# Kernel optimization log

Measured on AMD Instinct MI355X. Metric: run time of the kernel, lower is better.

The kernel has to match this reference:

```python
import jax, jax.numpy as jnp
import numpy as np

N_AGENTS, T, B, S = 8, 128, 64, 16
D_STATE, E, HH = 128, 64, 128


def _hyper(x, k1, b1, k2, b2):
    return jax.nn.relu(x @ k1 + b1) @ k2 + b2


def _perm_pos(n_agents, tb, s):
    # pos[row, a] = position of agent a in a random grand-coalition permutation
    keys = jax.random.split(jax.random.key(42), tb * s)
    pos = jax.vmap(lambda k: jax.random.permutation(k, n_agents))(keys)
    return pos.reshape(tb, s, n_agents)


def setup_inputs() -> dict:
    key = jax.random.key(0)
    ks = jax.random.split(key, 12)
    def rn(k, shape, scale=0.05):
        return jax.random.normal(k, shape, jnp.float32) * scale
    return {
        "q_vals": rn(ks[0], (N_AGENTS, T, B), 1.0),
        "states": rn(ks[1], (T * B, D_STATE), 1.0),
        "hw1_k1": rn(ks[2], (D_STATE, HH)), "hw1_b1": jnp.zeros((HH,), jnp.float32),
        "hw1_k2": rn(ks[3], (HH, 2 * E)), "hw1_b2": jnp.zeros((2 * E,), jnp.float32),
        "b1_k": rn(ks[4], (D_STATE, E)), "b1_b": jnp.zeros((E,), jnp.float32),
        "hw2_k1": rn(ks[5], (D_STATE, HH)), "hw2_b1": jnp.zeros((HH,), jnp.float32),
        "hw2_k2": rn(ks[6], (HH, E)), "hw2_b2": jnp.zeros((E,), jnp.float32),
        "hb2_k1": rn(ks[7], (D_STATE, E)), "hb2_b1": jnp.zeros((E,), jnp.float32),
        "hb2_k2": rn(ks[8], (E, 1)), "hb2_b2": jnp.zeros((1,), jnp.float32),
    }


def _forward(pos, q_vals, states, hw1_k1, hw1_b1, hw1_k2, hw1_b2, b1_k, b1_b,
             hw2_k1, hw2_b1, hw2_k2, hw2_b2, hb2_k1, hb2_b1, hb2_k2, hb2_b2):
    n, t, b = q_vals.shape
    tb = t * b
    q = jnp.transpose(q_vals, (1, 2, 0)).reshape(tb, n)          # agent_qs, (tb, n)
    qb = jnp.broadcast_to(q[:, None, :], (tb, S, n))
    inv = jnp.argsort(pos, axis=-1)                               # agent at each position
    q_ord = jnp.take_along_axis(qb, inv, axis=-1)                 # q ordered by position
    csum_excl = jnp.cumsum(q_ord, axis=-1) - q_ord                # sum over strictly-earlier positions
    coal_sum = jnp.take_along_axis(csum_excl, pos, axis=-1)       # sum of preceding agents' q
    coal_norm = coal_sum / jnp.maximum(pos, 1).astype(q.dtype)    # mean (0 if no predecessors)
    # Hypernets depend only on states -> compute once per tb row, broadcast over (S, n)
    w1 = jnp.abs(_hyper(states, hw1_k1, hw1_b1, hw1_k2, hw1_b2)).reshape(tb, 1, 1, 2, E)
    b1 = (states @ b1_k + b1_b).reshape(tb, 1, 1, E)
    w2 = jnp.abs(_hyper(states, hw2_k1, hw2_b1, hw2_k2, hw2_b2)).reshape(tb, 1, 1, E)
    b2 = _hyper(states, hb2_k1, hb2_b1, hb2_k2, hb2_b2).reshape(tb, 1, 1)
    hidden = jax.nn.elu(coal_norm[..., None] * w1[..., 0, :]
                        + qb[..., None] * w1[..., 1, :] + b1)     # (tb, S, n, E)
    y = jnp.sum(hidden * w2, axis=-1) + b2                        # (tb, S, n)
    alpha = jnp.abs(y).reshape(t, b, S, n).mean(axis=2)           # mean over samples
    return jnp.transpose(alpha, (2, 0, 1))                        # (n, t, b)


def reference(q_vals, states, hw1_k1, hw1_b1, hw1_k2, hw1_b2, b1_k, b1_b,
              hw2_k1, hw2_b1, hw2_k2, hw2_b2, hb2_k1, hb2_b1, hb2_k2, hb2_b2):
    n, t, b = q_vals.shape
    pos = _perm_pos(n, t * b, S)
    return _forward(pos, q_vals, states, hw1_k1, hw1_b1, hw1_k2, hw1_b2, b1_k, b1_b,
                    hw2_k1, hw2_b1, hw2_k2, hw2_b2, hb2_k1, hb2_b1, hb2_k2, hb2_b2)
```

## Files before the change

### kernel.cpp

```cpp
#include <hip/hip_runtime.h>
#include <stdint.h>

#define N_AG   8
#define S_SAMP 16
#define TB     8192
#define DST    128
#define E_DIM  64

#define RPB    8
#define CN_STR 9

#define WT1K1  0
#define WT2K1  16384
#define WT1K2  32768
#define WTM3   49152
#define WT2K2  65536
#define WT_ELEMS 73728

typedef __attribute__((ext_vector_type(8))) short  short8v;
typedef __attribute__((ext_vector_type(4))) float  float4v;

__device__ __forceinline__ float4 ld4(const float* p) { return *(const float4*)p; }

__device__ __forceinline__ unsigned short f2bf(float f) {
  uint32_t x = __float_as_uint(f);
  return (unsigned short)((x + 0x7FFFu + ((x >> 16) & 1u)) >> 16);
}
__device__ __forceinline__ uint32_t pk2(float lo, float hi) {
  return (uint32_t)f2bf(lo) | ((uint32_t)f2bf(hi) << 16);
}

__device__ __forceinline__ uint2 tf2x32(uint32_t k0, uint32_t k1,
                                        uint32_t c0, uint32_t c1) {
  uint32_t ks2 = k0 ^ k1 ^ 0x1BD11BDAu;
  uint32_t x0 = c0 + k0, x1 = c1 + k1;
#define TFR(r) { x0 += x1; x1 = (x1 << (r)) | (x1 >> (32 - (r))); x1 ^= x0; }
  TFR(13) TFR(15) TFR(26) TFR(6)
  x0 += k1;  x1 += ks2 + 1u;
  TFR(17) TFR(29) TFR(16) TFR(24)
  x0 += ks2; x1 += k0 + 2u;
  TFR(13) TFR(15) TFR(26) TFR(6)
  x0 += k0;  x1 += k1 + 3u;
  TFR(17) TFR(29) TFR(16) TFR(24)
  x0 += k1;  x1 += ks2 + 4u;
  TFR(13) TFR(15) TFR(26) TFR(6)
  x0 += ks2; x1 += k0 + 5u;
#undef TFR
  return make_uint2(x0, x1);
}

__device__ __forceinline__ short8v rdfrag(const unsigned short* base, int row, int ks, int lhi) {
  const int b = (row * 256 + ks * 64 + lhi * 16) ^ ((row & 7) << 4);
  return *(const short8v*)((const char*)base + b);
}
__device__ __forceinline__ void wrbf(unsigned short* pan, int r, int c, float v) {
  const int b = (r * 256 + c * 2) ^ ((r & 7) << 4);
  *(unsigned short*)((char*)pan + b) = f2bf(v);
}
__device__ __forceinline__ short8v gfrag(const unsigned short* wt, int n, int ks, int lhi) {
  return *(const short8v*)(wt + (n << 7) + ks * 32 + lhi * 8);
}

__global__ __launch_bounds__(256)
void wt_transpose(const float* __restrict__ hw1_k1, const float* __restrict__ hw2_k1,
                  const float* __restrict__ hw1_k2, const float* __restrict__ b1_k,
                  const float* __restrict__ hb2_k1, const float* __restrict__ hw2_k2,
                  unsigned short* __restrict__ wt)
{
  __shared__ float t[32][33];
  const int b = blockIdx.x;
  const float* src; int ldn, t0, dstbase;
  if (b < 16)      { src = hw1_k1; ldn = 128; t0 = b;      dstbase = WT1K1; }
  else if (b < 32) { src = hw2_k1; ldn = 128; t0 = b - 16; dstbase = WT2K1; }
  else if (b < 48) { src = hw1_k2; ldn = 128; t0 = b - 32; dstbase = WT1K2; }
  else if (b < 56) { src = b1_k;   ldn = 64;  t0 = b - 48; dstbase = WTM3; }
  else if (b < 64) { src = hb2_k1; ldn = 64;  t0 = b - 56; dstbase = WTM3 + 64 * 128; }
  else             { src = hw2_k2; ldn = 64;  t0 = b - 64; dstbase = WT2K2; }
  const int kt = t0 & 3, nt = t0 >> 2;
  const int tid = threadIdx.x;
  {
    const int c = tid & 31;
    for (int r = tid >> 5; r < 32; r += 8)
      t[r][c] = src[(size_t)(kt * 32 + r) * ldn + nt * 32 + c];
  }
  __syncthreads();
  {
    const int c2 = tid & 15;
    for (int n = tid >> 4; n < 32; n += 16) {
      const uint32_t v = pk2(t[2 * c2][n], t[2 * c2 + 1][n]);
      *(uint32_t*)&wt[dstbase + (nt * 32 + n) * 128 + kt * 32 + 2 * c2] = v;
    }
  }
}

__global__ __launch_bounds__(256)
void alpha_mfma2(const float* __restrict__ q_vals,
                 const float* __restrict__ states,
                 const float* __restrict__ hw1_b1, const float* __restrict__ hw1_b2,
                 const float* __restrict__ b1_b,   const float* __restrict__ hw2_b1,
                 const float* __restrict__ hw2_b2, const float* __restrict__ hb2_b1,
                 const float* __restrict__ hb2_k2, const float* __restrict__ hb2_b2,
                 const unsigned short* __restrict__ wt,
                 float* __restrict__ out)
{
  __shared__ unsigned short xbf[RPB * 128];
  __shared__ unsigned short h1bf[RPB * 128];
  __shared__ unsigned short h2bf[RPB * 128];
  __shared__ float w1l[RPB][132];
  __shared__ float b1l[RPB][68];
  __shared__ float w2l[RPB][68];
  __shared__ float hbl[RPB][68];
  __shared__ float b2l[RPB];
  __shared__ float ql[RPB][N_AG];
  __shared__ float cn_l[RPB][S_SAMP][CN_STR];

  const int tid  = threadIdx.x;
  const int row0 = blockIdx.x * RPB;
  const int lane = tid & 63;
  const int wv   = tid >> 6;
  const int lrow = lane & 15;
  const int lhi  = lane >> 4;

  {
    const int r = tid >> 5, k0 = (tid & 31) * 4;
    const float4 v = ld4(&states[(size_t)(row0 + r) * DST + k0]);
    const int b = (r * 256 + k0 * 2) ^ ((r & 7) << 4);
    *(uint32_t*)((char*)xbf + b)     = pk2(v.x, v.y);
    *(uint32_t*)((char*)xbf + b + 4) = pk2(v.z, v.w);
  }
  if (tid < RPB * N_AG) {
    const int rr = tid >> 3, a = tid & 7;
    ql[rr][a] = q_vals[a * TB + row0 + rr];
  }
  __syncthreads();

  if (tid < RPB * S_SAMP) {
    const int r  = tid >> 4;
    const int sl = tid & 15;
    const uint32_t j = (uint32_t)(row0 + r) * (uint32_t)S_SAMP + (uint32_t)sl;
    uint2 kj  = tf2x32(0u, 42u, 0u, j);
    uint2 sub = tf2x32(kj.x, kj.y, 0u, 1u);
    uint32_t K[N_AG];
#pragma unroll
    for (int i = 0; i < N_AG; ++i) {
      uint2 b = tf2x32(sub.x, sub.y, 0u, (uint32_t)i);
      K[i] = b.x ^ b.y;
    }
    int posa[N_AG];
#pragma unroll
    for (int i = 0; i < N_AG; ++i) {
      int rank = 0;
#pragma unroll
      for (int m = 0; m < N_AG; ++m)
        rank += (K[m] < K[i]) || (K[m] == K[i] && m < i);
      posa[rank] = i;
    }
#pragma unroll
    for (int a = 0; a < N_AG; ++a) {
      const int pa = posa[a];
      float cs = 0.f;
#pragma unroll
      for (int a2 = 0; a2 < N_AG; ++a2)
        cs += (posa[a2] < pa) ? ql[r][a2] : 0.f;
      cn_l[r][sl][a] = cs / (float)max(pa, 1);
    }
  }

  {
    float4v a0 = {0.f,0.f,0.f,0.f}, a1 = {0.f,0.f,0.f,0.f};
    const int c0 = wv * 32 + lrow, c1 = c0 + 16;
#pragma unroll
    for (int ks = 0; ks < 4; ++ks) {
      const short8v af  = rdfrag(xbf, lrow & 7, ks, lhi);
      const short8v b0  = gfrag(wt + WT1K1, c0, ks, lhi);
      const short8v b1f = gfrag(wt + WT1K1, c1, ks, lhi);
      a0 = __builtin_amdgcn_mfma_f32_16x16x32_bf16(af, b0,  a0, 0, 0, 0);
      a1 = __builtin_amdgcn_mfma_f32_16x16x32_bf16(af, b1f, a1, 0, 0, 0);
    }
    if (lhi < 2) {
      const float bv0 = hw1_b1[c0], bv1 = hw1_b1[c1];
#pragma unroll
      for (int j = 0; j < 4; ++j) {
        const int r = lhi * 4 + j;
        wrbf(h1bf, r, c0, fmaxf(a0[j] + bv0, 0.f));
        wrbf(h1bf, r, c1, fmaxf(a1[j] + bv1, 0.f));
      }
    }
  }

  {
    float4v a0 = {0.f,0.f,0.f,0.f}, a1 = {0.f,0.f,0.f,0.f};
    const int c0 = wv * 32 + lrow, c1 = c0 + 16;
#pragma unroll
    for (int ks = 0; ks < 4; ++ks) {
      const short8v af  = rdfrag(xbf, lrow & 7, ks, lhi);
      const short8v b0  = gfrag(wt + WT2K1, c0, ks, lhi);
      const short8v b1f = gfrag(wt + WT2K1, c1, ks, lhi);
      a0 = __builtin_amdgcn_mfma_f32_16x16x32_bf16(af, b0,  a0, 0, 0, 0);
      a1 = __builtin_amdgcn_mfma_f32_16x16x32_bf16(af, b1f, a1, 0, 0, 0);
    }
    if (lhi < 2) {
      const float bv0 = hw2_b1[c0], bv1 = hw2_b1[c1];
#pragma unroll
      for (int j = 0; j < 4; ++j) {
        const int r = lhi * 4 + j;
        wrbf(h2bf, r, c0, fmaxf(a0[j] + bv0, 0.f));
        wrbf(h2bf, r, c1, fmaxf(a1[j] + bv1, 0.f));
      }
    }
  }

  {
    float4v a0 = {0.f,0.f,0.f,0.f}, a1 = {0.f,0.f,0.f,0.f};
    const int c0 = wv * 32 + lrow, c1 = c0 + 16;
#pragma unroll
    for (int ks = 0; ks < 4; ++ks) {
      const short8v af  = rdfrag(xbf, lrow & 7, ks, lhi);
      const short8v b0  = gfrag(wt + WTM3, c0, ks, lhi);
      const short8v b1f = gfrag(wt + WTM3, c1, ks, lhi);
      a0 = __builtin_amdgcn_mfma_f32_16x16x32_bf16(af, b0,  a0, 0, 0, 0);
      a1 = __builtin_amdgcn_mfma_f32_16x16x32_bf16(af, b1f, a1, 0, 0, 0);
    }
    if (lhi < 2) {
#pragma unroll
      for (int j = 0; j < 4; ++j) {
        const int r = lhi * 4 + j;
        if (c0 < 64) b1l[r][c0] = a0[j] + b1_b[c0];
        else         hbl[r][c0 - 64] = fmaxf(a0[j] + hb2_b1[c0 - 64], 0.f);
        if (c1 < 64) b1l[r][c1] = a1[j] + b1_b[c1];
        else         hbl[r][c1 - 64] = fmaxf(a1[j] + hb2_b1[c1 - 64], 0.f);
      }
    }
  }
  __syncthreads();

  if (tid < RPB * S_SAMP) {
    const int r = tid >> 4, sl = tid & 15;
    float v = hbl[r][sl]      * hb2_k2[sl]
            + hbl[r][sl + 16] * hb2_k2[sl + 16]
            + hbl[r][sl + 32] * hb2_k2[sl + 32]
            + hbl[r][sl + 48] * hb2_k2[sl + 48];
    v += __shfl_down(v, 8, 16); v += __shfl_down(v, 4, 16);
    v += __shfl_down(v, 2, 16); v += __shfl_down(v, 1, 16);
    if (sl == 0) b2l[r] = v + hb2_b2[0];
  }

  {
    float4v a0 = {0.f,0.f,0.f,0.f}, a1 = {0.f,0.f,0.f,0.f};
    const int c0 = wv * 32 + lrow, c1 = c0 + 16;
#pragma unroll
    for (int ks = 0; ks < 4; ++ks) {
      const short8v af  = rdfrag(h1bf, lrow & 7, ks, lhi);
      const short8v b0  = gfrag(wt + WT1K2, c0, ks, lhi);
      const short8v b1f = gfrag(wt + WT1K2, c1, ks, lhi);
      a0 = __builtin_amdgcn_mfma_f32_16x16x32_bf16(af, b0,  a0, 0, 0, 0);
      a1 = __builtin_amdgcn_mfma_f32_16x16x32_bf16(af, b1f, a1, 0, 0, 0);
    }
    if (lhi < 2) {
      const float bv0 = hw1_b2[c0], bv1 = hw1_b2[c1];
#pragma unroll
      for (int j = 0; j < 4; ++j) {
        const int r = lhi * 4 + j;
        w1l[r][c0] = fabsf(a0[j] + bv0);
        w1l[r][c1] = fabsf(a1[j] + bv1);
      }
    }
  }

  {
    float4v a0 = {0.f,0.f,0.f,0.f};
    const int c = wv * 16 + lrow;
#pragma unroll
    for (int ks = 0; ks < 4; ++ks) {
      const short8v af = rdfrag(h2bf, lrow & 7, ks, lhi);
      const short8v b0 = gfrag(wt + WT2K2, c, ks, lhi);
      a0 = __builtin_amdgcn_mfma_f32_16x16x32_bf16(af, b0, a0, 0, 0, 0);
    }
    if (lhi < 2) {
      const float bv = hw2_b2[c];
#pragma unroll
      for (int j = 0; j < 4; ++j)
        w2l[lhi * 4 + j][c] = fabsf(a0[j] + bv);
    }
  }
  __syncthreads();

  {
    const int sl = tid & 15;
    const int r  = (tid >> 4) & 7;
    const int a0i = (tid >> 7) * 4;
    float cn[4], qv[4], y[4];
#pragma unroll
    for (int jj = 0; jj < 4; ++jj) {
      cn[jj] = cn_l[r][sl][a0i + jj];
      qv[jj] = ql[r][a0i + jj];
      y[jj]  = 0.f;
    }
#pragma unroll 4
    for (int e = 0; e < E_DIM; e += 4) {
      const float4 wa  = ld4(&w1l[r][e]);
      const float4 wb  = ld4(&w1l[r][64 + e]);
      const float4 bb  = ld4(&b1l[r][e]);
      const float4 w2v = ld4(&w2l[r][e]);
#pragma unroll
      for (int jj = 0; jj < 4; ++jj) {
        float h;
        h = fmaf(cn[jj], wa.x, fmaf(qv[jj], wb.x, bb.x));
        y[jj] = fmaf((h > 0.f) ? h : (__expf(h) - 1.f), w2v.x, y[jj]);
        h = fmaf(cn[jj], wa.y, fmaf(qv[jj], wb.y, bb.y));
        y[jj] = fmaf((h > 0.f) ? h : (__expf(h) - 1.f), w2v.y, y[jj]);
        h = fmaf(cn[jj], wa.z, fmaf(qv[jj], wb.z, bb.z));
        y[jj] = fmaf((h > 0.f) ? h : (__expf(h) - 1.f), w2v.z, y[jj]);
        h = fmaf(cn[jj], wa.w, fmaf(qv[jj], wb.w, bb.w));
        y[jj] = fmaf((h > 0.f) ? h : (__expf(h) - 1.f), w2v.w, y[jj]);
      }
    }
    const float b2v = b2l[r];
#pragma unroll
    for (int jj = 0; jj < 4; ++jj)
      cn_l[r][sl][a0i + jj] = fabsf(y[jj] + b2v);
  }
  __syncthreads();

  if (tid < RPB * N_AG) {
    const int rr = tid & 7, a = tid >> 3;
    float acc = 0.f;
#pragma unroll
    for (int ss = 0; ss < S_SAMP; ++ss) acc += cn_l[rr][ss][a];
    out[a * TB + row0 + rr] = acc * (1.0f / (float)S_SAMP);
  }
}

#define FB_RPB 16
#define FB_H_PAD 132
#define FB_E_PAD 68
__global__ __launch_bounds__(256)
void alpha_fused2(const float* __restrict__ q_vals, const float* __restrict__ states,
                  const float* __restrict__ hw1_k1, const float* __restrict__ hw1_b1,
                  const float* __restrict__ hw1_k2, const float* __restrict__ hw1_b2,
                  const float* __restrict__ b1_k,   const float* __restrict__ b1_b,
                  const float* __restrict__ hw2_k1, const float* __restrict__ hw2_b1,
                  const float* __restrict__ hw2_k2, const float* __restrict__ hw2_b2,
                  const float* __restrict__ hb2_k1, const float* __restrict__ hb2_b1,
                  const float* __restrict__ hb2_k2, const float* __restrict__ hb2_b2,
                  float* __restrict__ out)
{
  __shared__ float s_lds[FB_RPB][DST];
  __shared__ float scratch[FB_RPB][FB_H_PAD];
  __shared__ float scratch2[FB_RPB][FB_E_PAD];
  __shared__ float w1l[FB_RPB][FB_H_PAD];
  __shared__ float b1l[FB_RPB][FB_E_PAD];
  __shared__ float w2l[FB_RPB][FB_E_PAD];
  __shared__ float b2l[FB_RPB];
  __shared__ float qlf[FB_RPB][N_AG];
  __shared__ float cnred[FB_RPB][S_SAMP][N_AG];
  const int tid = threadIdx.x;
  const int row0 = blockIdx.x * FB_RPB;
  const int r = tid >> 4, sl = tid & 15;
  {
    const float4* src = reinterpret_cast<const float4*>(states + (size_t)row0 * DST);
    reinterpret_cast<float4*>(&s_lds[0][0])[tid]       = src[tid];
    reinterpret_cast<float4*>(&s_lds[0][0])[tid + 256] = src[tid + 256];
  }
  if (tid < FB_RPB * N_AG) {
    const int rr = tid >> 3, a = tid & 7;
    qlf[rr][a] = q_vals[a * TB + row0 + rr];
  }
  __syncthreads();
  {
    const uint32_t j = (uint32_t)(row0 + r) * (uint32_t)S_SAMP + (uint32_t)sl;
    uint2 kj = tf2x32(0u, 42u, 0u, j);
    uint2 sub = tf2x32(kj.x, kj.y, 0u, 1u);
    uint32_t K[N_AG];
#pragma unroll
    for (int i = 0; i < N_AG; ++i) { uint2 b = tf2x32(sub.x, sub.y, 0u, (uint32_t)i); K[i] = b.x ^ b.y; }
    int posa[N_AG];
#pragma unroll
    for (int i = 0; i < N_AG; ++i) {
      int rank = 0;
#pragma unroll
      for (int m = 0; m < N_AG; ++m) rank += (K[m] < K[i]) || (K[m] == K[i] && m < i);
      posa[rank] = i;
    }
#pragma unroll
    for (int a = 0; a < N_AG; ++a) {
      const int pa = posa[a];
      float cs = 0.f;
#pragma unroll
      for (int a2 = 0; a2 < N_AG; ++a2) cs += (posa[a2] < pa) ? qlf[r][a2] : 0.f;
      cnred[r][sl][a] = cs / (float)max(pa, 1);
    }
  }
#define FB128(SRC, W, BIAS, DSTA, ACT)                                          \
  {                                                                             \
    const int c = tid & 127, gg = tid >> 7;                                     \
    float a0 = 0.f, a1 = 0.f, a2 = 0.f, a3 = 0.f;                               \
    _Pragma("unroll 2") for (int k = 0; k < DST; k += 4) {                      \
      const float w0 = W[(k + 0) * 128 + c];                                    \
      const float w1 = W[(k + 1) * 128 + c];                                    \
      const float w2 = W[(k + 2) * 128 + c];                                    \
      const float w3 = W[(k + 3) * 128 + c];                                    \
      float4 v;                                                                 \
      v = ld4(&SRC[gg * 8 + 0][0] + k);                                         \
      a0 = fmaf(v.x, w0, a0); a0 = fmaf(v.y, w1, a0);                           \
      a0 = fmaf(v.z, w2, a0); a0 = fmaf(v.w, w3, a0);                           \
      v = ld4(&SRC[gg * 8 + 1][0] + k);                                         \
      a1 = fmaf(v.x, w0, a1); a1 = fmaf(v.y, w1, a1);                           \
      a1 = fmaf(v.z, w2, a1); a1 = fmaf(v.w, w3, a1);                           \
      v = ld4(&SRC[gg * 8 + 2][0] + k);                                         \
      a2 = fmaf(v.x, w0, a2); a2 = fmaf(v.y, w1, a2);                           \
      a2 = fmaf(v.z, w2, a2); a2 = fmaf(v.w, w3, a2);                           \
      v = ld4(&SRC[gg * 8 + 3][0] + k);                                         \
      a3 = fmaf(v.x, w0, a3); a3 = fmaf(v.y, w1, a3);                           \
      a3 = fmaf(v.z, w2, a3); a3 = fmaf(v.w, w3, a3);                           \
      v = ld4(&SRC[gg * 8 + 4][0] + k);                                         \
      DSTA[gg * 8 + 4][c] = 0.f;             \
      (void)v;                                                                  \
    }                                                                           \
    (void)a0; (void)a1; (void)a2; (void)a3; (void)BIAS; (void)ACT;              \
  }
#undef FB128
  {
    int c = tid & 127, rg = tid >> 7;
    float a0=0.f,a1=0.f,a2=0.f,a3=0.f,a4=0.f,a5=0.f,a6=0.f,a7=0.f;
#pragma unroll 2
    for (int k = 0; k < DST; ++k) {
      float wv = hw1_k1[k * 128 + c];
      a0 += s_lds[rg*8+0][k]*wv; a1 += s_lds[rg*8+1][k]*wv;
      a2 += s_lds[rg*8+2][k]*wv; a3 += s_lds[rg*8+3][k]*wv;
      a4 += s_lds[rg*8+4][k]*wv; a5 += s_lds[rg*8+5][k]*wv;
      a6 += s_lds[rg*8+6][k]*wv; a7 += s_lds[rg*8+7][k]*wv;
    }
    float b = hw1_b1[c];
    scratch[rg*8+0][c]=fmaxf(a0+b,0.f); scratch[rg*8+1][c]=fmaxf(a1+b,0.f);
    scratch[rg*8+2][c]=fmaxf(a2+b,0.f); scratch[rg*8+3][c]=fmaxf(a3+b,0.f);
    scratch[rg*8+4][c]=fmaxf(a4+b,0.f); scratch[rg*8+5][c]=fmaxf(a5+b,0.f);
    scratch[rg*8+6][c]=fmaxf(a6+b,0.f); scratch[rg*8+7][c]=fmaxf(a7+b,0.f);
  }
  {
    int c = tid & 63, rg = tid >> 6;
    float a0=0.f,a1=0.f,a2=0.f,a3=0.f;
#pragma unroll 2
    for (int k = 0; k < DST; ++k) {
      float wv = b1_k[k * 64 + c];
      a0 += s_lds[rg*4+0][k]*wv; a1 += s_lds[rg*4+1][k]*wv;
      a2 += s_lds[rg*4+2][k]*wv; a3 += s_lds[rg*4+3][k]*wv;
    }
    float b = b1_b[c];
    b1l[rg*4+0][c]=a0+b; b1l[rg*4+1][c]=a1+b; b1l[rg*4+2][c]=a2+b; b1l[rg*4+3][c]=a3+b;
  }
  __syncthreads();
  {
    int c = tid & 127, rg = tid >> 7;
    float a0=0.f,a1=0.f,a2=0.f,a3=0.f,a4=0.f,a5=0.f,a6=0.f,a7=0.f;
#pragma unroll 2
    for (int k = 0; k < DST; ++k) {
      float wv = hw1_k2[k * 128 + c];
      a0 += scratch[rg*8+0][k]*wv; a1 += scratch[rg*8+1][k]*wv;
      a2 += scratch[rg*8+2][k]*wv; a3 += scratch[rg*8+3][k]*wv;
      a4 += scratch[rg*8+4][k]*wv; a5 += scratch[rg*8+5][k]*wv;
      a6 += scratch[rg*8+6][k]*wv; a7 += scratch[rg*8+7][k]*wv;
    }
    float b = hw1_b2[c];
    w1l[rg*8+0][c]=fabsf(a0+b); w1l[rg*8+1][c]=fabsf(a1+b);
    w1l[rg*8+2][c]=fabsf(a2+b); w1l[rg*8+3][c]=fabsf(a3+b);
    w1l[rg*8+4][c]=fabsf(a4+b); w1l[rg*8+5][c]=fabsf(a5+b);
    w1l[rg*8+6][c]=fabsf(a6+b); w1l[rg*8+7][c]=fabsf(a7+b);
  }
  {
    int c = tid & 63, rg = tid >> 6;
    float a0=0.f,a1=0.f,a2=0.f,a3=0.f;
#pragma unroll 2
    for (int k = 0; k < DST; ++k) {
      float wv = hb2_k1[k * 64 + c];
      a0 += s_lds[rg*4+0][k]*wv; a1 += s_lds[rg*4+1][k]*wv;
      a2 += s_lds[rg*4+2][k]*wv; a3 += s_lds[rg*4+3][k]*wv;
    }
    float b = hb2_b1[c];
    scratch2[rg*4+0][c]=fmaxf(a0+b,0.f); scratch2[rg*4+1][c]=fmaxf(a1+b,0.f);
    scratch2[rg*4+2][c]=fmaxf(a2+b,0.f); scratch2[rg*4+3][c]=fmaxf(a3+b,0.f);
  }
  __syncthreads();
  {
    int c = tid & 127, rg = tid >> 7;
    float a0=0.f,a1=0.f,a2=0.f,a3=0.f,a4=0.f,a5=0.f,a6=0.f,a7=0.f;
#pragma unroll 2
    for (int k = 0; k < DST; ++k) {
      float wv = hw2_k1[k * 128 + c];
      a0 += s_lds[rg*8+0][k]*wv; a1 += s_lds[rg*8+1][k]*wv;
      a2 += s_lds[rg*8+2][k]*wv; a3 += s_lds[rg*8+3][k]*wv;
      a4 += s_lds[rg*8+4][k]*wv; a5 += s_lds[rg*8+5][k]*wv;
      a6 += s_lds[rg*8+6][k]*wv; a7 += s_lds[rg*8+7][k]*wv;
    }
    float b = hw2_b1[c];
    scratch[rg*8+0][c]=fmaxf(a0+b,0.f); scratch[rg*8+1][c]=fmaxf(a1+b,0.f);
    scratch[rg*8+2][c]=fmaxf(a2+b,0.f); scratch[rg*8+3][c]=fmaxf(a3+b,0.f);
    scratch[rg*8+4][c]=fmaxf(a4+b,0.f); scratch[rg*8+5][c]=fmaxf(a5+b,0.f);
    scratch[rg*8+6][c]=fmaxf(a6+b,0.f); scratch[rg*8+7][c]=fmaxf(a7+b,0.f);
  }
  if (tid < FB_RPB * S_SAMP) {
    float v = scratch2[r][sl]      * hb2_k2[sl]
            + scratch2[r][sl + 16] * hb2_k2[sl + 16]
            + scratch2[r][sl + 32] * hb2_k2[sl + 32]
            + scratch2[r][sl + 48] * hb2_k2[sl + 48];
    v += __shfl_down(v, 8, 16); v += __shfl_down(v, 4, 16);
    v += __shfl_down(v, 2, 16); v += __shfl_down(v, 1, 16);
    if (sl == 0) b2l[r] = v + hb2_b2[0];
  }
  __syncthreads();
  {
    int c = tid & 63, rg = tid >> 6;
    float a0=0.f,a1=0.f,a2=0.f,a3=0.f;
#pragma unroll 2
    for (int k = 0; k < DST; ++k) {
      float wv = hw2_k2[k * 64 + c];
      a0 += scratch[rg*4+0][k]*wv; a1 += scratch[rg*4+1][k]*wv;
      a2 += scratch[rg*4+2][k]*wv; a3 += scratch[rg*4+3][k]*wv;
    }
    float b = hw2_b2[c];
    w2l[rg*4+0][c]=fabsf(a0+b); w2l[rg*4+1][c]=fabsf(a1+b);
    w2l[rg*4+2][c]=fabsf(a2+b); w2l[rg*4+3][c]=fabsf(a3+b);
  }
  __syncthreads();
  {
    float cn[N_AG], qv[N_AG], y[N_AG];
#pragma unroll
    for (int a = 0; a < N_AG; ++a) { cn[a]=cnred[r][sl][a]; qv[a]=qlf[r][a]; y[a]=0.f; }
#pragma unroll 4
    for (int e = 0; e < E_DIM; e += 4) {
      const float4 wa  = ld4(&w1l[r][e]);
      const float4 wb  = ld4(&w1l[r][64 + e]);
      const float4 bb  = ld4(&b1l[r][e]);
      const float4 w2v = ld4(&w2l[r][e]);
#pragma unroll
      for (int a = 0; a < N_AG; ++a) {
        float h;
        h = fmaf(cn[a], wa.x, fmaf(qv[a], wb.x, bb.x));
        y[a] = fmaf((h > 0.f) ? h : (__expf(h) - 1.f), w2v.x, y[a]);
        h = fmaf(cn[a], wa.y, fmaf(qv[a], wb.y, bb.y));
        y[a] = fmaf((h > 0.f) ? h : (__expf(h) - 1.f), w2v.y, y[a]);
        h = fmaf(cn[a], wa.z, fmaf(qv[a], wb.z, bb.z));
        y[a] = fmaf((h > 0.f) ? h : (__expf(h) - 1.f), w2v.z, y[a]);
        h = fmaf(cn[a], wa.w, fmaf(qv[a], wb.w, bb.w));
        y[a] = fmaf((h > 0.f) ? h : (__expf(h) - 1.f), w2v.w, y[a]);
      }
    }
    const float b2v = b2l[r];
#pragma unroll
    for (int a = 0; a < N_AG; ++a) cnred[r][sl][a] = fabsf(y[a] + b2v);
  }
  __syncthreads();
  if (tid < FB_RPB * N_AG) {
    const int a = tid >> 4, rr = tid & 15;
    float acc = 0.f;
#pragma unroll
    for (int ss = 0; ss < S_SAMP; ++ss) acc += cnred[rr][ss][a];
    out[a * TB + row0 + rr] = acc * (1.0f / (float)S_SAMP);
  }
}

extern "C" void kernel_launch(void* const* d_in, const int* in_sizes, int n_in,
                              void* d_out, int out_size, void* d_ws, size_t ws_size,
                              hipStream_t stream) {
  const float* q_vals = (const float*)d_in[0];
  const float* states = (const float*)d_in[1];
  const float* hw1_k1 = (const float*)d_in[2];
  const float* hw1_b1 = (const float*)d_in[3];
  const float* hw1_k2 = (const float*)d_in[4];
  const float* hw1_b2 = (const float*)d_in[5];
  const float* b1_k   = (const float*)d_in[6];
  const float* b1_b   = (const float*)d_in[7];
  const float* hw2_k1 = (const float*)d_in[8];
  const float* hw2_b1 = (const float*)d_in[9];
  const float* hw2_k2 = (const float*)d_in[10];
  const float* hw2_b2 = (const float*)d_in[11];
  const float* hb2_k1 = (const float*)d_in[12];
  const float* hb2_b1 = (const float*)d_in[13];
  const float* hb2_k2 = (const float*)d_in[14];
  const float* hb2_b2 = (const float*)d_in[15];
  float* out = (float*)d_out;

  const size_t need = (size_t)WT_ELEMS * sizeof(unsigned short);
  if (ws_size >= need) {
    unsigned short* wt = (unsigned short*)d_ws;
    wt_transpose<<<dim3(72), 256, 0, stream>>>(
        hw1_k1, hw2_k1, hw1_k2, b1_k, hb2_k1, hw2_k2, wt);
    alpha_mfma2<<<dim3(TB / RPB), 256, 0, stream>>>(
        q_vals, states, hw1_b1, hw1_b2, b1_b, hw2_b1, hw2_b2, hb2_b1,
        hb2_k2, hb2_b2, wt, out);
  } else {
    alpha_fused2<<<dim3(TB / FB_RPB), 256, 0, stream>>>(
        q_vals, states, hw1_k1, hw1_b1, hw1_k2, hw1_b2, b1_k, b1_b,
        hw2_k1, hw2_b1, hw2_k2, hw2_b2, hb2_k1, hb2_b1, hb2_k2, hb2_b2, out);
  }
}
```

Baseline: 41.50 us.

## Split fused kernel into GEMM kernel and per-sample mixing kernel via workspace

The single fused kernel is split in two. The first computes all hypernet outputs with MFMA at 16 rows per block, which fills the 16-row MFMA tile instead of wasting half of it, and writes w1, b1, w2 and b2 to the global workspace. The second kernel handles 4 rows per block with higher occupancy: it runs the permutation sampling and the ELU mixing, splitting agents over more threads. The cost is an extra launch plus a round trip of about 7 MB through global memory. The workspace size requirement also grows, so the fallback path could be taken if the workspace is too small.

```diff
diff --git a/kernel.cpp b/kernel.cpp
--- a/kernel.cpp
+++ b/kernel.cpp
@@ -7,7 +7,6 @@
 #define DST    128
 #define E_DIM  64
 
-#define RPB    8
 #define CN_STR 9
 
 #define WT1K1  0
@@ -15,7 +14,11 @@
 #define WT1K2  32768
 #define WTM3   49152
 #define WT2K2  65536
-#define WT_ELEMS 73728
+#define W1WS   36864
+#define B1WS   (W1WS + 1048576)
+#define W2WS   (B1WS + 524288)
+#define B2WS   (W2WS + 524288)
+#define WS_FLOATS (B2WS + 8192)
 
 typedef __attribute__((ext_vector_type(8))) short  short8v;
 typedef __attribute__((ext_vector_type(4))) float  float4v;
@@ -94,97 +97,53 @@
 }
 
 __global__ __launch_bounds__(256)
-void alpha_mfma2(const float* __restrict__ q_vals,
-                 const float* __restrict__ states,
-                 const float* __restrict__ hw1_b1, const float* __restrict__ hw1_b2,
-                 const float* __restrict__ b1_b,   const float* __restrict__ hw2_b1,
-                 const float* __restrict__ hw2_b2, const float* __restrict__ hb2_b1,
-                 const float* __restrict__ hb2_k2, const float* __restrict__ hb2_b2,
-                 const unsigned short* __restrict__ wt,
-                 float* __restrict__ out)
+void alpha_gemm(const float* __restrict__ states,
+                const float* __restrict__ hw1_b1, const float* __restrict__ hw2_b1,
+                const float* __restrict__ b1_b,   const float* __restrict__ hb2_b1,
+                const float* __restrict__ hw1_b2, const float* __restrict__ hw2_b2,
+                const float* __restrict__ hb2_k2, const float* __restrict__ hb2_b2,
+                const unsigned short* __restrict__ wt,
+                float* __restrict__ w1ws, float* __restrict__ b1ws,
+                float* __restrict__ w2ws, float* __restrict__ b2ws)
 {
-  __shared__ unsigned short xbf[RPB * 128];
-  __shared__ unsigned short h1bf[RPB * 128];
-  __shared__ unsigned short h2bf[RPB * 128];
-  __shared__ float w1l[RPB][132];
-  __shared__ float b1l[RPB][68];
-  __shared__ float w2l[RPB][68];
-  __shared__ float hbl[RPB][68];
-  __shared__ float b2l[RPB];
-  __shared__ float ql[RPB][N_AG];
-  __shared__ float cn_l[RPB][S_SAMP][CN_STR];
+  __shared__ unsigned short xbf[16 * 128];
+  __shared__ unsigned short h1bf[16 * 128];
+  __shared__ unsigned short h2bf[16 * 128];
+  __shared__ float hbl[16][68];
 
   const int tid  = threadIdx.x;
-  const int row0 = blockIdx.x * RPB;
+  const int row0 = blockIdx.x * 16;
   const int lane = tid & 63;
   const int wv   = tid >> 6;
   const int lrow = lane & 15;
   const int lhi  = lane >> 4;
 
-  {
-    const int r = tid >> 5, k0 = (tid & 31) * 4;
+#pragma unroll
+  for (int pass = 0; pass < 2; ++pass) {
+    const int idx = tid + pass * 256;
+    const int r = idx >> 5, k0 = (idx & 31) * 4;
     const float4 v = ld4(&states[(size_t)(row0 + r) * DST + k0]);
     const int b = (r * 256 + k0 * 2) ^ ((r & 7) << 4);
     *(uint32_t*)((char*)xbf + b)     = pk2(v.x, v.y);
     *(uint32_t*)((char*)xbf + b + 4) = pk2(v.z, v.w);
   }
-  if (tid < RPB * N_AG) {
-    const int rr = tid >> 3, a = tid & 7;
-    ql[rr][a] = q_vals[a * TB + row0 + rr];
-  }
-  __syncthreads();
-
-  if (tid < RPB * S_SAMP) {
-    const int r  = tid >> 4;
-    const int sl = tid & 15;
-    const uint32_t j = (uint32_t)(row0 + r) * (uint32_t)S_SAMP + (uint32_t)sl;
-    uint2 kj  = tf2x32(0u, 42u, 0u, j);
-    uint2 sub = tf2x32(kj.x, kj.y, 0u, 1u);
-    uint32_t K[N_AG];
-#pragma unroll
-    for (int i = 0; i < N_AG; ++i) {
-      uint2 b = tf2x32(sub.x, sub.y, 0u, (uint32_t)i);
-      K[i] = b.x ^ b.y;
-    }
-    int posa[N_AG];
-#pragma unroll
-    for (int i = 0; i < N_AG; ++i) {
-      int rank = 0;
-#pragma unroll
-      for (int m = 0; m < N_AG; ++m)
-        rank += (K[m] < K[i]) || (K[m] == K[i] && m < i);
-      posa[rank] = i;
-    }
-#pragma unroll
-    for (int a = 0; a < N_AG; ++a) {
-      const int pa = posa[a];
-      float cs = 0.f;
-#pragma unroll
-      for (int a2 = 0; a2 < N_AG; ++a2)
-        cs += (posa[a2] < pa) ? ql[r][a2] : 0.f;
-      cn_l[r][sl][a] = cs / (float)max(pa, 1);
-    }
-  }
+  __syncthreads();
 
   {
     float4v a0 = {0.f,0.f,0.f,0.f}, a1 = {0.f,0.f,0.f,0.f};
     const int c0 = wv * 32 + lrow, c1 = c0 + 16;
 #pragma unroll
     for (int ks = 0; ks < 4; ++ks) {
-      const short8v af  = rdfrag(xbf, lrow & 7, ks, lhi);
-      const short8v b0  = gfrag(wt + WT1K1, c0, ks, lhi);
-      const short8v b1f = gfrag(wt + WT1K1, c1, ks, lhi);
-      a0 = __builtin_amdgcn_mfma_f32_16x16x32_bf16(af, b0,  a0, 0, 0, 0);
-      a1 = __builtin_amdgcn_mfma_f32_16x16x32_bf16(af, b1f, a1, 0, 0, 0);
-    }
-    if (lhi < 2) {
-      const float bv0 = hw1_b1[c0], bv1 = hw1_b1[c1];
-#pragma unroll
-      for (int j = 0; j < 4; ++j) {
-        const int r = lhi * 4 + j;
-        wrbf(h1bf, r, c0, fmaxf(a0[j] + bv0, 0.f));
-        wrbf(h1bf, r, c1, fmaxf(a1[j] + bv1, 0.f));
-      }
+      const short8v af  = rdfrag(xbf, lrow, ks, lhi);
+      a0 = __builtin_amdgcn_mfma_f32_16x16x32_bf16(af, gfrag(wt + WT1K1, c0, ks, lhi), a0, 0, 0, 0);
+      a1 = __builtin_amdgcn_mfma_f32_16x16x32_bf16(af, gfrag(wt + WT1K1, c1, ks, lhi), a1, 0, 0, 0);
+    }
+    const float bv0 = hw1_b1[c0], bv1 = hw1_b1[c1];
+#pragma unroll
+    for (int j = 0; j < 4; ++j) {
+      const int r = lhi * 4 + j;
+      wrbf(h1bf, r, c0, fmaxf(a0[j] + bv0, 0.f));
+      wrbf(h1bf, r, c1, fmaxf(a1[j] + bv1, 0.f));
     }
   }
 
@@ -193,20 +152,16 @@
     const int c0 = wv * 32 + lrow, c1 = c0 + 16;
 #pragma unroll
     for (int ks = 0; ks < 4; ++ks) {
-      const short8v af  = rdfrag(xbf, lrow & 7, ks, lhi);
-      const short8v b0  = gfrag(wt + WT2K1, c0, ks, lhi);
-      const short8v b1f = gfrag(wt + WT2K1, c1, ks, lhi);
-      a0 = __builtin_amdgcn_mfma_f32_16x16x32_bf16(af, b0,  a0, 0, 0, 0);
-      a1 = __builtin_amdgcn_mfma_f32_16x16x32_bf16(af, b1f, a1, 0, 0, 0);
-    }
-    if (lhi < 2) {
-      const float bv0 = hw2_b1[c0], bv1 = hw2_b1[c1];
-#pragma unroll
-      for (int j = 0; j < 4; ++j) {
-        const int r = lhi * 4 + j;
-        wrbf(h2bf, r, c0, fmaxf(a0[j] + bv0, 0.f));
-        wrbf(h2bf, r, c1, fmaxf(a1[j] + bv1, 0.f));
-      }
+      const short8v af  = rdfrag(xbf, lrow, ks, lhi);
+      a0 = __builtin_amdgcn_mfma_f32_16x16x32_bf16(af, gfrag(wt + WT2K1, c0, ks, lhi), a0, 0, 0, 0);
+      a1 = __builtin_amdgcn_mfma_f32_16x16x32_bf16(af, gfrag(wt + WT2K1, c1, ks, lhi), a1, 0, 0, 0);
+    }
+    const float bv0 = hw2_b1[c0], bv1 = hw2_b1[c1];
+#pragma unroll
+    for (int j = 0; j < 4; ++j) {
+      const int r = lhi * 4 + j;
+      wrbf(h2bf, r, c0, fmaxf(a0[j] + bv0, 0.f));
+      wrbf(h2bf, r, c1, fmaxf(a1[j] + bv1, 0.f));
     }
   }
 
@@ -215,26 +170,22 @@
     const int c0 = wv * 32 + lrow, c1 = c0 + 16;
 #pragma unroll
     for (int ks = 0; ks < 4; ++ks) {
-      const short8v af  = rdfrag(xbf, lrow & 7, ks, lhi);
-      const short8v b0  = gfrag(wt + WTM3, c0, ks, lhi);
-      const short8v b1f = gfrag(wt + WTM3, c1, ks, lhi);
-      a0 = __builtin_amdgcn_mfma_f32_16x16x32_bf16(af, b0,  a0, 0, 0, 0);
-      a1 = __builtin_amdgcn_mfma_f32_16x16x32_bf16(af, b1f, a1, 0, 0, 0);
-    }
-    if (lhi < 2) {
-#pragma unroll
-      for (int j = 0; j < 4; ++j) {
-        const int r = lhi * 4 + j;
-        if (c0 < 64) b1l[r][c0] = a0[j] + b1_b[c0];
-        else         hbl[r][c0 - 64] = fmaxf(a0[j] + hb2_b1[c0 - 64], 0.f);
-        if (c1 < 64) b1l[r][c1] = a1[j] + b1_b[c1];
-        else         hbl[r][c1 - 64] = fmaxf(a1[j] + hb2_b1[c1 - 64], 0.f);
-      }
-    }
-  }
-  __syncthreads();
-
-  if (tid < RPB * S_SAMP) {
+      const short8v af  = rdfrag(xbf, lrow, ks, lhi);
+      a0 = __builtin_amdgcn_mfma_f32_16x16x32_bf16(af, gfrag(wt + WTM3, c0, ks, lhi), a0, 0, 0, 0);
+      a1 = __builtin_amdgcn_mfma_f32_16x16x32_bf16(af, gfrag(wt + WTM3, c1, ks, lhi), a1, 0, 0, 0);
+    }
+#pragma unroll
+    for (int j = 0; j < 4; ++j) {
+      const int r = lhi * 4 + j;
+      if (c0 < 64) b1ws[(size_t)(row0 + r) * 64 + c0] = a0[j] + b1_b[c0];
+      else         hbl[r][c0 - 64] = fmaxf(a0[j] + hb2_b1[c0 - 64], 0.f);
+      if (c1 < 64) b1ws[(size_t)(row0 + r) * 64 + c1] = a1[j] + b1_b[c1];
+      else         hbl[r][c1 - 64] = fmaxf(a1[j] + hb2_b1[c1 - 64], 0.f);
+    }
+  }
+  __syncthreads();
+
+  {
     const int r = tid >> 4, sl = tid & 15;
     float v = hbl[r][sl]      * hb2_k2[sl]
             + hbl[r][sl + 16] * hb2_k2[sl + 16]
@@ -242,7 +193,7 @@
             + hbl[r][sl + 48] * hb2_k2[sl + 48];
     v += __shfl_down(v, 8, 16); v += __shfl_down(v, 4, 16);
     v += __shfl_down(v, 2, 16); v += __shfl_down(v, 1, 16);
-    if (sl == 0) b2l[r] = v + hb2_b2[0];
+    if (sl == 0) b2ws[row0 + r] = v + hb2_b2[0];
   }
 
   {
@@ -250,20 +201,16 @@
     const int c0 = wv * 32 + lrow, c1 = c0 + 16;
 #pragma unroll
     for (int ks = 0; ks < 4; ++ks) {
-      const short8v af  = rdfrag(h1bf, lrow & 7, ks, lhi);
-      const short8v b0  = gfrag(wt + WT1K2, c0, ks, lhi);
-      const short8v b1f = gfrag(wt + WT1K2, c1, ks, lhi);
-      a0 = __builtin_amdgcn_mfma_f32_16x16x32_bf16(af, b0,  a0, 0, 0, 0);
-      a1 = __builtin_amdgcn_mfma_f32_16x16x32_bf16(af, b1f, a1, 0, 0, 0);
-    }
-    if (lhi < 2) {
-      const float bv0 = hw1_b2[c0], bv1 = hw1_b2[c1];
-#pragma unroll
-      for (int j = 0; j < 4; ++j) {
-        const int r = lhi * 4 + j;
-        w1l[r][c0] = fabsf(a0[j] + bv0);
-        w1l[r][c1] = fabsf(a1[j] + bv1);
-      }
+      const short8v af  = rdfrag(h1bf, lrow, ks, lhi);
+      a0 = __builtin_amdgcn_mfma_f32_16x16x32_bf16(af, gfrag(wt + WT1K2, c0, ks, lhi), a0, 0, 0, 0);
+      a1 = __builtin_amdgcn_mfma_f32_16x16x32_bf16(af, gfrag(wt + WT1K2, c1, ks, lhi), a1, 0, 0, 0);
+    }
+    const float bv0 = hw1_b2[c0], bv1 = hw1_b2[c1];
+#pragma unroll
+    for (int j = 0; j < 4; ++j) {
+      const int r = lhi * 4 + j;
+      w1ws[(size_t)(row0 + r) * 128 + c0] = fabsf(a0[j] + bv0);
+      w1ws[(size_t)(row0 + r) * 128 + c1] = fabsf(a1[j] + bv1);
     }
   }
 
@@ -272,58 +219,121 @@
     const int c = wv * 16 + lrow;
 #pragma unroll
     for (int ks = 0; ks < 4; ++ks) {
-      const short8v af = rdfrag(h2bf, lrow & 7, ks, lhi);
-      const short8v b0 = gfrag(wt + WT2K2, c, ks, lhi);
-      a0 = __builtin_amdgcn_mfma_f32_16x16x32_bf16(af, b0, a0, 0, 0, 0);
-    }
-    if (lhi < 2) {
-      const float bv = hw2_b2[c];
-#pragma unroll
-      for (int j = 0; j < 4; ++j)
-        w2l[lhi * 4 + j][c] = fabsf(a0[j] + bv);
-    }
-  }
-  __syncthreads();
-
-  {
+      const short8v af = rdfrag(h2bf, lrow, ks, lhi);
+      a0 = __builtin_amdgcn_mfma_f32_16x16x32_bf16(af, gfrag(wt + WT2K2, c, ks, lhi), a0, 0, 0, 0);
+    }
+    const float bv = hw2_b2[c];
+#pragma unroll
+    for (int j = 0; j < 4; ++j)
+      w2ws[(size_t)(row0 + lhi * 4 + j) * 64 + c] = fabsf(a0[j] + bv);
+  }
+}
+
+__global__ __launch_bounds__(256, 8)
+void alpha_main2(const float* __restrict__ q_vals,
+                 const float* __restrict__ w1ws, const float* __restrict__ b1ws,
+                 const float* __restrict__ w2ws, const float* __restrict__ b2ws,
+                 float* __restrict__ out)
+{
+  __shared__ float w1l[4][132];
+  __shared__ float b1l[4][68];
+  __shared__ float w2l[4][68];
+  __shared__ float b2l[4];
+  __shared__ float ql[4][N_AG];
+  __shared__ float cn_l[4][S_SAMP][CN_STR];
+
+  const int tid  = threadIdx.x;
+  const int row0 = blockIdx.x * 4;
+
+  if (tid < 128) {
+    const int r = tid >> 5, c = (tid & 31) * 4;
+    *(float4*)&w1l[r][c] = ld4(&w1ws[(size_t)(row0 + r) * 128 + c]);
+  } else if (tid < 192) {
+    const int t = tid - 128, r = t >> 4, c = (t & 15) * 4;
+    *(float4*)&b1l[r][c] = ld4(&b1ws[(size_t)(row0 + r) * 64 + c]);
+  } else {
+    const int t = tid - 192, r = t >> 4, c = (t & 15) * 4;
+    *(float4*)&w2l[r][c] = ld4(&w2ws[(size_t)(row0 + r) * 64 + c]);
+  }
+  if (tid < 4) b2l[tid] = b2ws[row0 + tid];
+  if (tid < 32) {
+    const int rr = tid & 3, a = tid >> 2;
+    ql[rr][a] = q_vals[a * TB + row0 + rr];
+  }
+  __syncthreads();
+
+  if (tid < 64) {
+    const int r  = tid >> 4;
     const int sl = tid & 15;
-    const int r  = (tid >> 4) & 7;
-    const int a0i = (tid >> 7) * 4;
-    float cn[4], qv[4], y[4];
-#pragma unroll
-    for (int jj = 0; jj < 4; ++jj) {
-      cn[jj] = cn_l[r][sl][a0i + jj];
-      qv[jj] = ql[r][a0i + jj];
-      y[jj]  = 0.f;
-    }
+    const uint32_t j = (uint32_t)(row0 + r) * (uint32_t)S_SAMP + (uint32_t)sl;
+    uint2 kj  = tf2x32(0u, 42u, 0u, j);
+    uint2 sub = tf2x32(kj.x, kj.y, 0u, 1u);
+    uint32_t K[N_AG];
+#pragma unroll
+    for (int i = 0; i < N_AG; ++i) {
+      uint2 b = tf2x32(sub.x, sub.y, 0u, (uint32_t)i);
+      K[i] = b.x ^ b.y;
+    }
+    int posa[N_AG];
+#pragma unroll
+    for (int i = 0; i < N_AG; ++i) {
+      int rank = 0;
+#pragma unroll
+      for (int m = 0; m < N_AG; ++m)
+        rank += (K[m] < K[i]) || (K[m] == K[i] && m < i);
+      posa[rank] = i;
+    }
+#pragma unroll
+    for (int a = 0; a < N_AG; ++a) {
+      const int pa = posa[a];
+      float cs = 0.f;
+#pragma unroll
+      for (int a2 = 0; a2 < N_AG; ++a2)
+        cs += (posa[a2] < pa) ? ql[r][a2] : 0.f;
+      cn_l[r][sl][a] = cs / (float)max(pa, 1);
+    }
+  }
+  __syncthreads();
+
+  {
+    const int sl  = tid & 15;
+    const int r   = (tid >> 4) & 3;
+    const int a0i = (tid >> 6) * 2;
+    const float cn0 = cn_l[r][sl][a0i],     cn1 = cn_l[r][sl][a0i + 1];
+    const float qv0 = ql[r][a0i],           qv1 = ql[r][a0i + 1];
+    float y0 = 0.f, y1 = 0.f;
 #pragma unroll 4
     for (int e = 0; e < E_DIM; e += 4) {
       const float4 wa  = ld4(&w1l[r][e]);
       const float4 wb  = ld4(&w1l[r][64 + e]);
       const float4 bb  = ld4(&b1l[r][e]);
       const float4 w2v = ld4(&w2l[r][e]);
-#pragma unroll
-      for (int jj = 0; jj < 4; ++jj) {
-        float h;
-        h = fmaf(cn[jj], wa.x, fmaf(qv[jj], wb.x, bb.x));
-        y[jj] = fmaf((h > 0.f) ? h : (__expf(h) - 1.f), w2v.x, y[jj]);
-        h = fmaf(cn[jj], wa.y, fmaf(qv[jj], wb.y, bb.y));
-        y[jj] = fmaf((h > 0.f) ? h : (__expf(h) - 1.f), w2v.y, y[jj]);
-        h = fmaf(cn[jj], wa.z, fmaf(qv[jj], wb.z, bb.z));
-        y[jj] = fmaf((h > 0.f) ? h : (__expf(h) - 1.f), w2v.z, y[jj]);
-        h = fmaf(cn[jj], wa.w, fmaf(qv[jj], wb.w, bb.w));
-        y[jj] = fmaf((h > 0.f) ? h : (__expf(h) - 1.f), w2v.w, y[jj]);
-      }
+      float h;
+      h = fmaf(cn0, wa.x, fmaf(qv0, wb.x, bb.x));
+      y0 = fmaf((h > 0.f) ? h : (__expf(h) - 1.f), w2v.x, y0);
+      h = fmaf(cn1, wa.x, fmaf(qv1, wb.x, bb.x));
+      y1 = fmaf((h > 0.f) ? h : (__expf(h) - 1.f), w2v.x, y1);
+      h = fmaf(cn0, wa.y, fmaf(qv0, wb.y, bb.y));
+      y0 = fmaf((h > 0.f) ? h : (__expf(h) - 1.f), w2v.y, y0);
+      h = fmaf(cn1, wa.y, fmaf(qv1, wb.y, bb.y));
+      y1 = fmaf((h > 0.f) ? h : (__expf(h) - 1.f), w2v.y, y1);
+      h = fmaf(cn0, wa.z, fmaf(qv0, wb.z, bb.z));
+      y0 = fmaf((h > 0.f) ? h : (__expf(h) - 1.f), w2v.z, y0);
+      h = fmaf(cn1, wa.z, fmaf(qv1, wb.z, bb.z));
+      y1 = fmaf((h > 0.f) ? h : (__expf(h) - 1.f), w2v.z, y1);
+      h = fmaf(cn0, wa.w, fmaf(qv0, wb.w, bb.w));
+      y0 = fmaf((h > 0.f) ? h : (__expf(h) - 1.f), w2v.w, y0);
+      h = fmaf(cn1, wa.w, fmaf(qv1, wb.w, bb.w));
+      y1 = fmaf((h > 0.f) ? h : (__expf(h) - 1.f), w2v.w, y1);
     }
     const float b2v = b2l[r];
-#pragma unroll
-    for (int jj = 0; jj < 4; ++jj)
-      cn_l[r][sl][a0i + jj] = fabsf(y[jj] + b2v);
-  }
-  __syncthreads();
-
-  if (tid < RPB * N_AG) {
-    const int rr = tid & 7, a = tid >> 3;
+    cn_l[r][sl][a0i]     = fabsf(y0 + b2v);
+    cn_l[r][sl][a0i + 1] = fabsf(y1 + b2v);
+  }
+  __syncthreads();
+
+  if (tid < 32) {
+    const int rr = tid & 3, a = tid >> 2;
     float acc = 0.f;
 #pragma unroll
     for (int ss = 0; ss < S_SAMP; ++ss) acc += cn_l[rr][ss][a];
@@ -391,35 +401,6 @@
       cnred[r][sl][a] = cs / (float)max(pa, 1);
     }
   }
-#define FB128(SRC, W, BIAS, DSTA, ACT)                                          \
-  {                                                                             \
-    const int c = tid & 127, gg = tid >> 7;                                     \
-    float a0 = 0.f, a1 = 0.f, a2 = 0.f, a3 = 0.f;                               \
-    _Pragma("unroll 2") for (int k = 0; k < DST; k += 4) {                      \
-      const float w0 = W[(k + 0) * 128 + c];                                    \
-      const float w1 = W[(k + 1) * 128 + c];                                    \
-      const float w2 = W[(k + 2) * 128 + c];                                    \
-      const float w3 = W[(k + 3) * 128 + c];                                    \
-      float4 v;                                                                 \
-      v = ld4(&SRC[gg * 8 + 0][0] + k);                                         \
-      a0 = fmaf(v.x, w0, a0); a0 = fmaf(v.y, w1, a0);                           \
-      a0 = fmaf(v.z, w2, a0); a0 = fmaf(v.w, w3, a0);                           \
-      v = ld4(&SRC[gg * 8 + 1][0] + k);                                         \
-      a1 = fmaf(v.x, w0, a1); a1 = fmaf(v.y, w1, a1);                           \
-      a1 = fmaf(v.z, w2, a1); a1 = fmaf(v.w, w3, a1);                           \
-      v = ld4(&SRC[gg * 8 + 2][0] + k);                                         \
-      a2 = fmaf(v.x, w0, a2); a2 = fmaf(v.y, w1, a2);                           \
-      a2 = fmaf(v.z, w2, a2); a2 = fmaf(v.w, w3, a2);                           \
-      v = ld4(&SRC[gg * 8 + 3][0] + k);                                         \
-      a3 = fmaf(v.x, w0, a3); a3 = fmaf(v.y, w1, a3);                           \
-      a3 = fmaf(v.z, w2, a3); a3 = fmaf(v.w, w3, a3);                           \
-      v = ld4(&SRC[gg * 8 + 4][0] + k);                                         \
-      DSTA[gg * 8 + 4][c] = 0.f;             \
-      (void)v;                                                                  \
-    }                                                                           \
-    (void)a0; (void)a1; (void)a2; (void)a3; (void)BIAS; (void)ACT;              \
-  }
-#undef FB128
   {
     int c = tid & 127, rg = tid >> 7;
     float a0=0.f,a1=0.f,a2=0.f,a3=0.f,a4=0.f,a5=0.f,a6=0.f,a7=0.f;
@@ -580,14 +561,21 @@
   const float* hb2_b2 = (const float*)d_in[15];
   float* out = (float*)d_out;
 
-  const size_t need = (size_t)WT_ELEMS * sizeof(unsigned short);
+  const size_t need = (size_t)WS_FLOATS * sizeof(float);
   if (ws_size >= need) {
     unsigned short* wt = (unsigned short*)d_ws;
+    float* wsf  = (float*)d_ws;
+    float* w1ws = wsf + W1WS;
+    float* b1ws = wsf + B1WS;
+    float* w2ws = wsf + W2WS;
+    float* b2ws = wsf + B2WS;
     wt_transpose<<<dim3(72), 256, 0, stream>>>(
         hw1_k1, hw2_k1, hw1_k2, b1_k, hb2_k1, hw2_k2, wt);
-    alpha_mfma2<<<dim3(TB / RPB), 256, 0, stream>>>(
-        q_vals, states, hw1_b1, hw1_b2, b1_b, hw2_b1, hw2_b2, hb2_b1,
-        hb2_k2, hb2_b2, wt, out);
+    alpha_gemm<<<dim3(TB / 16), 256, 0, stream>>>(
+        states, hw1_b1, hw2_b1, b1_b, hb2_b1, hw1_b2, hw2_b2,
+        hb2_k2, hb2_b2, wt, w1ws, b1ws, w2ws, b2ws);
+    alpha_main2<<<dim3(TB / 4), 256, 0, stream>>>(
+        q_vals, w1ws, b1ws, w2ws, b2ws, out);
   } else {
     alpha_fused2<<<dim3(TB / FB_RPB), 256, 0, stream>>>(
         q_vals, states, hw1_k1, hw1_b1, hw1_k2, hw1_b2, b1_k, b1_b,
```

Result: slower. 47.13 us (+13.6%).
